# Kernel optimization log

Measured on AMD Instinct MI355X. Metric: run time of the kernel, lower is better.

The kernel has to match this reference:

```python
import jax, jax.numpy as jnp
import numpy as np
import math

# (mul, l, parity) triples for irreps_in1 == irreps_in2 == '32x0e+16x1o+8x2e'
IRREPS = [(32, 0, 1), (16, 1, -1), (8, 2, 1)]
BATCH = 2048


def _fact(n):
    return math.factorial(n)


def _w3j_entry(j1, j2, j3, m1, m2, m3):
    # Racah formula for the (complex-basis) Wigner 3j symbol, integer l's.
    if m1 + m2 + m3 != 0:
        return 0.0
    t_min = max(0, j2 - j3 - m1, j1 - j3 + m2)
    t_max = min(j1 + j2 - j3, j1 - m1, j2 + m2)
    if t_max < t_min:
        return 0.0
    s = 0.0
    for t in range(t_min, t_max + 1):
        s += (-1) ** t / (
            _fact(t) * _fact(j3 - j2 + t + m1) * _fact(j3 - j1 + t - m2)
            * _fact(j1 + j2 - j3 - t) * _fact(j1 - t - m1) * _fact(j2 - t + m2))
    delta = math.sqrt(_fact(j1 + j2 - j3) * _fact(j1 - j2 + j3)
                      * _fact(-j1 + j2 + j3) / _fact(j1 + j2 + j3 + 1))
    pref = math.sqrt(_fact(j1 + m1) * _fact(j1 - m1) * _fact(j2 + m2)
                     * _fact(j2 - m2) * _fact(j3 + m3) * _fact(j3 - m3))
    return (-1) ** (j1 - j2 - m3) * delta * pref * s


def _w3j_complex(j1, j2, j3):
    W = np.zeros((2 * j1 + 1, 2 * j2 + 1, 2 * j3 + 1))
    for m1 in range(-j1, j1 + 1):
        for m2 in range(-j2, j2 + 1):
            m3 = -(m1 + m2)
            if abs(m3) <= j3:
                W[m1 + j1, m2 + j2, m3 + j3] = _w3j_entry(j1, j2, j3, m1, m2, m3)
    return W


def _c2r(l):
    # complex -> real spherical harmonic change-of-basis (rows: real m, cols: complex mu)
    U = np.zeros((2 * l + 1, 2 * l + 1), dtype=np.complex128)
    U[l, l] = 1.0
    rs2 = 1.0 / math.sqrt(2.0)
    for m in range(1, l + 1):
        U[l + m, l + m] = (-1) ** m * rs2
        U[l + m, l - m] = rs2
        U[l - m, l - m] = 1j * rs2
        U[l - m, l + m] = -1j * (-1) ** m * rs2
    return U


def _w3j_real(l1, l2, l3):
    # Wigner 3j in the real spherical-harmonic basis (same sparsity/math as e3nn o3.wigner_3j)
    W = _w3j_complex(l1, l2, l3).astype(np.complex128)
    C = np.einsum('abc,ia,jb,kc->ijk', W, _c2r(l1), _c2r(l2), _c2r(l3))
    if np.linalg.norm(C.imag) > np.linalg.norm(C.real):
        C = np.ascontiguousarray(C.imag)
    else:
        C = np.ascontiguousarray(C.real)
    C[np.abs(C) < 1e-12] = 0.0
    return C


def _build_structure():
    # Mirrors CudaTensorProduct.__init__ with irreps_out=None: enumerate every
    # then emit sparse COO entries (in1_idx, in2_idx, out_idx, cb_val).
    entries_by_l3 = {}
    off1 = 0
    for mul1, l1, p1 in IRREPS:
        off2_base = 0
        for mul2, l2, p2 in IRREPS:
            for l3 in range(abs(l1 - l2), l1 + l2 + 1):
                p3 = (p1 * p2 + 1) // 2
                o1 = off1
                for _i in range(mul1):
                    o2 = off2_base
                    for _j in range(mul2):
                        entries_by_l3.setdefault((l3, p3), []).append((l1, l2, o1, o2))
                        o2 += 2 * l2 + 1
                    o1 += 2 * l1 + 1
            off2_base += (2 * l2 + 1) * mul2
        off1 += (2 * l1 + 1) * mul1

    l3s = sorted(entries_by_l3.keys(), key=lambda x: 2 * (x[0] + 1) + x[1])
    in1_idx, in2_idx, out_idx, cb_vals = [], [], [], []
    row = 0
    w3j_cache = {}
    for l3, p3 in l3s:
        for l1, l2, o1, o2 in entries_by_l3[(l3, p3)]:
            key = (l1, l2, l3)
            if key not in w3j_cache:
                w3j_cache[key] = _w3j_real(l1, l2, l3)
            C = w3j_cache[key]
            scale = math.sqrt(2 * l3 + 1)
            for m3 in range(2 * l3 + 1):
                for m2 in range(2 * l2 + 1):
                    for m1 in range(2 * l1 + 1):
                        v = C[m1, m2, m3]
                        if v == 0.0:
                            continue
                        in1_idx.append(m1 + o1)
                        in2_idx.append(m2 + o2)
                        out_idx.append(m3 + row)
                        cb_vals.append(float(v * scale))
            row += 2 * l3 + 1

    # palette/index encoding, as in the module (palette[0] == 0 is the filler slot)
    palette = sorted(set(cb_vals))
    palette.insert(0, 0.0)
    lut = {v: i for i, v in enumerate(palette)}
    cb_idx = [lut[v] for v in cb_vals]
    return (np.asarray(in1_idx, np.int32), np.asarray(in2_idx, np.int32),
            np.asarray(out_idx, np.int32), np.asarray(cb_idx, np.int32),
            np.asarray(palette, np.float32), row)


def setup_inputs() -> dict:
    key = jax.random.key(0)
    k1, k2 = jax.random.split(key)
    i1, i2, io, ic, pal, cb_height = _build_structure()
    dim = sum(m * (2 * l + 1) for m, l, _ in IRREPS)  # 120
    return {
        'in1': jax.random.normal(k1, (BATCH, dim), jnp.float32),
        'in2': jax.random.normal(k2, (BATCH, dim), jnp.float32),
        'cb_palette': jnp.asarray(pal),
        'in1_indices': jnp.asarray(i1),
        'in2_indices': jnp.asarray(i2),
        'out_indices': jnp.asarray(io),
        'cb_indices': jnp.asarray(ic),
        'cb_height': int(cb_height),
    }


def reference(in1, in2, cb_palette, in1_indices, in2_indices, out_indices, cb_indices, cb_height):
    # intermediate[b, o] = sum_k palette[cb_idx[k]] * in1[b, i1[k]] * in2[b, i2[k]]
    vals = cb_palette[cb_indices]                                   # [K]
    contrib = in1[:, in1_indices] * in2[:, in2_indices] * vals[None, :]  # [B, K]
    # scatter-accumulate along the sparse output rows
    out = jax.ops.segment_sum(contrib.T, out_indices, num_segments=cb_height).T  # [B, cb_height]
    return out
```

## Files before the change

### kernel.cpp

```cpp
#include <hip/hip_runtime.h>

#define DIM 120
#define NB 16
#define NBP 20
#define BLOCK 256
#define NG (NB / 4)
#define NXCD 8

__global__ void pre_kernel(const int* __restrict__ out_idx, int K, int H,
                           int* __restrict__ row_start,
                           const int* __restrict__ i1, const int* __restrict__ i2,
                           const int* __restrict__ cb, const float* __restrict__ pal,
                           uint2* __restrict__ ent) {
    int t = blockIdx.x * blockDim.x + threadIdx.x;
    if (t <= H) {
        int lo = 0, hi = K;
        while (lo < hi) {
            int mid = (lo + hi) >> 1;
            if (out_idx[mid] < t) lo = mid + 1; else hi = mid;
        }
        row_start[t] = lo;
    }
    if (t < K) {
        uint2 e;
        e.x = (unsigned)i1[t] | ((unsigned)i2[t] << 16);
        e.y = __float_as_uint(pal[cb[t]]);
        ent[t] = e;
    }
}

__global__ __launch_bounds__(BLOCK, 8) void tp_kernel(
    const float* __restrict__ in1, const float* __restrict__ in2,
    const uint2* __restrict__ ent, const int* __restrict__ row_start,
    float* __restrict__ out, int H, int nbx) {
    int x = blockIdx.x;
    {
        const int q = nbx / NXCD, r = nbx % NXCD;
        const int xcd = x % NXCD, pos = x / NXCD;
        x = (xcd < r) ? (xcd * (q + 1) + pos) : (r * (q + 1) + (xcd - r) * q + pos);
    }

    __shared__ __align__(16) float s1t[DIM * NBP];
    __shared__ __align__(16) float s2t[DIM * NBP];

    const int b0 = blockIdx.y * NB;
    for (int t = threadIdx.x; t < 2 * DIM * NG; t += BLOCK) {
        const int arr = (t >= DIM * NG);
        const int c = arr ? t - DIM * NG : t;
        const int d = c % DIM;
        const int g = c / DIM;
        const float* __restrict__ src = arr ? in2 : in1;
        const size_t base = (size_t)(b0 + 4 * g) * DIM + d;
        float4 v;
        v.x = src[base + 0 * DIM];
        v.y = src[base + 1 * DIM];
        v.z = src[base + 2 * DIM];
        v.w = src[base + 3 * DIM];
        float* dst = arr ? s2t : s1t;
        *(float4*)(dst + d * NBP + 4 * g) = v;
    }
    __syncthreads();

    const int o = x * BLOCK + threadIdx.x;
    if (o >= H) return;
    const int k0 = row_start[o];
    const int k1 = row_start[o + 1];

    float acc[NB];
#pragma unroll
    for (int b = 0; b < NB; ++b) acc[b] = 0.0f;

    for (int k = k0; k < k1; ++k) {
        const uint2 e = ent[k];
        const float4* __restrict__ pa = (const float4*)(s1t + (e.x & 0xffffu) * NBP);
        const float4* __restrict__ pc = (const float4*)(s2t + (e.x >> 16) * NBP);
        const float v = __uint_as_float(e.y);
#pragma unroll
        for (int j = 0; j < NG; ++j) {
            const float4 x4 = pa[j];
            const float4 y4 = pc[j];
            acc[4 * j + 0] = fmaf(v * x4.x, y4.x, acc[4 * j + 0]);
            acc[4 * j + 1] = fmaf(v * x4.y, y4.y, acc[4 * j + 1]);
            acc[4 * j + 2] = fmaf(v * x4.z, y4.z, acc[4 * j + 2]);
            acc[4 * j + 3] = fmaf(v * x4.w, y4.w, acc[4 * j + 3]);
        }
    }

#pragma unroll
    for (int b = 0; b < NB; ++b)
        out[(size_t)(b0 + b) * H + o] = acc[b];
}

extern "C" void kernel_launch(void* const* d_in, const int* in_sizes, int n_in,
                              void* d_out, int out_size, void* d_ws, size_t ws_size,
                              hipStream_t stream) {
    const float* in1 = (const float*)d_in[0];
    const float* in2 = (const float*)d_in[1];
    const float* pal = (const float*)d_in[2];
    const int*   i1  = (const int*)d_in[3];
    const int*   i2  = (const int*)d_in[4];
    const int*   oi  = (const int*)d_in[5];
    const int*   cb  = (const int*)d_in[6];

    const int K = in_sizes[3];
    const int B = in_sizes[0] / DIM;
    const int H = out_size / B;

    uint2* ent = (uint2*)d_ws;
    int* row_start = (int*)((char*)d_ws + (size_t)K * sizeof(uint2));

    {
        const int n = (K > H + 1) ? K : (H + 1);
        pre_kernel<<<(n + 255) / 256, 256, 0, stream>>>(oi, K, H, row_start,
                                                        i1, i2, cb, pal, ent);
    }

    const int nbx = (H + BLOCK - 1) / BLOCK;
    dim3 grid(nbx, B / NB);
    tp_kernel<<<grid, BLOCK, 0, stream>>>(in1, in2, ent, row_start,
                                          (float*)d_out, H, nbx);
}
```

Baseline: 33.31 us.

## Fuse preprocessing into main kernel, computing row bounds by in-kernel binary search

Removes the separate pre-kernel launch that built packed index entries and row offsets. Each thread now binary-searches out_indices for its row bounds, overlapped with the shared-memory staging, and reads i1, i2, cb and the palette directly in the inner loop. This saves a kernel launch and a workspace round trip. In exchange the main loop does more scattered global loads, including a dependent palette lookup, and every block in the batch dimension repeats the binary searches.

Measured after the change: 47.29 us. 1.42x slower.

```diff
diff --git a/kernel.cpp b/kernel.cpp
--- a/kernel.cpp
+++ b/kernel.cpp
@@ -7,32 +7,21 @@
 #define NG (NB / 4)
 #define NXCD 8
 
-__global__ void pre_kernel(const int* __restrict__ out_idx, int K, int H,
-                           int* __restrict__ row_start,
-                           const int* __restrict__ i1, const int* __restrict__ i2,
-                           const int* __restrict__ cb, const float* __restrict__ pal,
-                           uint2* __restrict__ ent) {
-    int t = blockIdx.x * blockDim.x + threadIdx.x;
-    if (t <= H) {
-        int lo = 0, hi = K;
-        while (lo < hi) {
-            int mid = (lo + hi) >> 1;
-            if (out_idx[mid] < t) lo = mid + 1; else hi = mid;
-        }
-        row_start[t] = lo;
+__device__ __forceinline__ int lower_bound(const int* __restrict__ a, int n, int v) {
+    int lo = 0, hi = n;
+    while (lo < hi) {
+        int m = (lo + hi) >> 1;
+        if (a[m] < v) lo = m + 1; else hi = m;
     }
-    if (t < K) {
-        uint2 e;
-        e.x = (unsigned)i1[t] | ((unsigned)i2[t] << 16);
-        e.y = __float_as_uint(pal[cb[t]]);
-        ent[t] = e;
-    }
+    return lo;
 }
 
 __global__ __launch_bounds__(BLOCK, 8) void tp_kernel(
     const float* __restrict__ in1, const float* __restrict__ in2,
-    const uint2* __restrict__ ent, const int* __restrict__ row_start,
-    float* __restrict__ out, int H, int nbx) {
+    const float* __restrict__ pal,
+    const int* __restrict__ i1, const int* __restrict__ i2,
+    const int* __restrict__ oi, const int* __restrict__ cb,
+    float* __restrict__ out, int H, int K, int nbx) {
     int x = blockIdx.x;
     {
         const int q = nbx / NXCD, r = nbx % NXCD;
@@ -42,6 +31,12 @@
 
     __shared__ __align__(16) float s1t[DIM * NBP];
     __shared__ __align__(16) float s2t[DIM * NBP];
+
+    const int o = x * BLOCK + (int)threadIdx.x;
+    const int om  = (o < H) ? o : H;
+    const int om1 = (o + 1 < H) ? o + 1 : H;
+    const int k0 = lower_bound(oi, K, om);
+    const int k1 = lower_bound(oi, K, om1);
 
     const int b0 = blockIdx.y * NB;
     for (int t = threadIdx.x; t < 2 * DIM * NG; t += BLOCK) {
@@ -61,20 +56,18 @@
     }
     __syncthreads();
 
-    const int o = x * BLOCK + threadIdx.x;
     if (o >= H) return;
-    const int k0 = row_start[o];
-    const int k1 = row_start[o + 1];
 
     float acc[NB];
 #pragma unroll
     for (int b = 0; b < NB; ++b) acc[b] = 0.0f;
 
     for (int k = k0; k < k1; ++k) {
-        const uint2 e = ent[k];
-        const float4* __restrict__ pa = (const float4*)(s1t + (e.x & 0xffffu) * NBP);
-        const float4* __restrict__ pc = (const float4*)(s2t + (e.x >> 16) * NBP);
-        const float v = __uint_as_float(e.y);
+        const int a = i1[k];
+        const int c = i2[k];
+        const float v = pal[cb[k]];
+        const float4* __restrict__ pa = (const float4*)(s1t + a * NBP);
+        const float4* __restrict__ pc = (const float4*)(s2t + c * NBP);
 #pragma unroll
         for (int j = 0; j < NG; ++j) {
             const float4 x4 = pa[j];
@@ -106,17 +99,8 @@
     const int B = in_sizes[0] / DIM;
     const int H = out_size / B;
 
-    uint2* ent = (uint2*)d_ws;
-    int* row_start = (int*)((char*)d_ws + (size_t)K * sizeof(uint2));
-
-    {
-        const int n = (K > H + 1) ? K : (H + 1);
-        pre_kernel<<<(n + 255) / 256, 256, 0, stream>>>(oi, K, H, row_start,
-                                                        i1, i2, cb, pal, ent);
-    }
-
     const int nbx = (H + BLOCK - 1) / BLOCK;
     dim3 grid(nbx, B / NB);
-    tp_kernel<<<grid, BLOCK, 0, stream>>>(in1, in2, ent, row_start,
-                                          (float*)d_out, H, nbx);
+    tp_kernel<<<grid, BLOCK, 0, stream>>>(in1, in2, pal, i1, i2, oi, cb,
+                                          (float*)d_out, H, K, nbx);
 }
```
